# Performance work log

Hardware: AMD Instinct MI355X
Metric: run time of the kernel (lower is better)

The kernel has to match this reference:

```python
import jax, jax.numpy as jnp
import numpy as np

U = 100000   # num_users
I = 50000    # num_items
N = U + I    # total nodes
D = 64       # embed_size
L = 3        # n_layers
E = 2000000  # num edges
EPS = 1e-12  # F.normalize default eps


def setup_inputs() -> dict:
    key = jax.random.key(0)
    k1, k2, k3, k4 = jax.random.split(key, 4)
    user_emb = jax.random.normal(k1, (U, D), dtype=jnp.float32) * 0.1
    item_emb = jax.random.normal(k2, (I, D), dtype=jnp.float32) * 0.1
    rows = jax.random.randint(k3, (E,), 0, N, dtype=jnp.int32)
    cols = jax.random.randint(k4, (E,), 0, N, dtype=jnp.int32)
    return {"user_emb": user_emb, "item_emb": item_emb, "rows": rows, "cols": cols}


def _spmm(vals, rows, cols, x):
    # sparse [N,N] @ dense [N,D] via gather + segment reduce
    return jax.ops.segment_sum(vals[:, None] * x[cols], rows, num_segments=N)


def _l2norm(x):
    return x / jnp.maximum(jnp.linalg.norm(x, axis=1, keepdims=True), EPS)


def reference(user_emb, item_emb, rows, cols):
    emb0 = jnp.concatenate([user_emb, item_emb], axis=0)  # [N, D]

    # laplacian_adj: G = D^-1/2 A D^-1/2 on the same edge set
    deg = jax.ops.segment_sum(jnp.ones((E,), emb0.dtype), rows, num_segments=N)
    d_is = jnp.where(deg > 0, deg ** -0.5, 0.0)
    g_vals = d_is[rows] * d_is[cols]  # [E]

    cur = emb0
    acc = emb0
    user_fine, item_fine = [], []
    for _ in range(L):
        gnn = _spmm(g_vals, rows, cols, cur)  # [N, D]
        # fine_laplacian_adj: cosine-sim edge scores, row-normalized
        gr = _l2norm(gnn[rows])
        gc = _l2norm(gnn[cols])
        scores = (jnp.sum(gr * gc, axis=1) + 1.0) * 0.5  # [E] in [0,1]
        rowsum = jax.ops.segment_sum(scores, rows, num_segments=N)
        d_inv = jnp.where(rowsum > 0, 1.0 / rowsum, 0.0)
        fine = _spmm(d_inv[rows] * scores, rows, cols, cur)  # [N, D]
        cur = gnn + fine
        acc = acc + cur
        user_fine.append(fine[:U])
        item_fine.append(fine[U:])

    u_embs = acc[:U]
    i_embs = acc[U:]
    return (u_embs, i_embs, jnp.stack(user_fine, 0), jnp.stack(item_fine, 0))
```

## Files before the change

### kernel.cpp

```cpp
#include <hip/hip_runtime.h>

namespace {

typedef unsigned short u16;
typedef __attribute__((__ext_vector_type__(2))) float f32x2;
typedef __attribute__((__ext_vector_type__(4))) float f32x4;

constexpr int Un = 100000;
constexpr int In = 50000;
constexpr int Nn = 150000;
constexpr int D  = 64;
constexpr int Ln = 3;
constexpr int En = 2000000;
constexpr int CHUNK = 1024;
constexpr int NB = (Nn + CHUNK - 1) / CHUNK;
constexpr int DCAP = 128;
constexpr int NW = Nn / 8;

__device__ __forceinline__ u16 f2bf(float f) {
    unsigned u = __float_as_uint(f);
    unsigned r = (u + 0x7FFFu + ((u >> 16) & 1u)) >> 16;
    return (u16)r;
}
__device__ __forceinline__ float bflo(unsigned u) {
    return __uint_as_float(u << 16);
}
__device__ __forceinline__ float bfhi(unsigned u) {
    return __uint_as_float(u & 0xFFFF0000u);
}
__device__ __forceinline__ unsigned pack2(float lo, float hi) {
    return (unsigned)f2bf(lo) | ((unsigned)f2bf(hi) << 16);
}

__device__ __forceinline__ f32x2 pkfma(f32x2 a, f32x2 b, f32x2 c) {
    f32x2 d;
    asm("v_pk_fma_f32 %0, %1, %2, %3" : "=v"(d) : "v"(a), "v"(b), "v"(c));
    return d;
}
__device__ __forceinline__ f32x2 pkadd(f32x2 a, f32x2 b) {
    f32x2 d;
    asm("v_pk_add_f32 %0, %1, %2" : "=v"(d) : "v"(a), "v"(b));
    return d;
}

__device__ __forceinline__ float dpp_add8(float x) {
    x += __uint_as_float((unsigned)__builtin_amdgcn_update_dpp(
        0, (int)__float_as_uint(x), 0xB1, 0xF, 0xF, true));
    x += __uint_as_float((unsigned)__builtin_amdgcn_update_dpp(
        0, (int)__float_as_uint(x), 0x4E, 0xF, 0xF, true));
    x += __uint_as_float((unsigned)__builtin_amdgcn_update_dpp(
        0, (int)__float_as_uint(x), 0x141, 0xF, 0xF, true));
    return x;
}

__device__ __forceinline__ void unp8(uint4 q, f32x2* o) {
    o[0].x = bflo(q.x); o[0].y = bfhi(q.x);
    o[1].x = bflo(q.y); o[1].y = bfhi(q.y);
    o[2].x = bflo(q.z); o[2].y = bfhi(q.z);
    o[3].x = bflo(q.w); o[3].y = bfhi(q.w);
}

__global__ void count_kernel(const int* __restrict__ rows, int* __restrict__ deg,
                             int* __restrict__ eoff) {
    int e = blockIdx.x * blockDim.x + threadIdx.x;
    if (e < En) eoff[e] = atomicAdd(&deg[rows[e]], 1);
}

__global__ void scan_partial(const int* __restrict__ deg, float* __restrict__ d_is,
                             int* __restrict__ bsum) {
    int tid = threadIdx.x;
    int base = blockIdx.x * CHUNK + tid * 4;
    int s = 0;
#pragma unroll
    for (int i = 0; i < 4; ++i) {
        int idx = base + i;
        if (idx < Nn) {
            int d = deg[idx];
            s += d;
            d_is[idx] = d > 0 ? rsqrtf((float)d) : 0.f;
        }
    }
    __shared__ int sh[256];
    sh[tid] = s;
    __syncthreads();
    for (int o = 128; o > 0; o >>= 1) {
        if (tid < o) sh[tid] += sh[tid + o];
        __syncthreads();
    }
    if (tid == 0) bsum[blockIdx.x] = sh[0];
}

__global__ void scan_top(int* __restrict__ bsum, int* __restrict__ row_ptr) {
    __shared__ int sh[256];
    int tid = threadIdx.x;
    int v = (tid < NB) ? bsum[tid] : 0;
    sh[tid] = v;
    __syncthreads();
    for (int o = 1; o < 256; o <<= 1) {
        int t = (tid >= o) ? sh[tid - o] : 0;
        __syncthreads();
        sh[tid] += t;
        __syncthreads();
    }
    if (tid < NB) bsum[tid] = sh[tid] - v;
    if (tid == 255) row_ptr[Nn] = sh[255];
}

__global__ void scan_final(const int* __restrict__ deg, const int* __restrict__ bsum,
                           int* __restrict__ row_ptr) {
    int tid = threadIdx.x;
    int base = blockIdx.x * CHUNK + tid * 4;
    int v[4];
    int ts = 0;
#pragma unroll
    for (int i = 0; i < 4; ++i) {
        int idx = base + i;
        v[i] = (idx < Nn) ? deg[idx] : 0;
        ts += v[i];
    }
    __shared__ int sh[256];
    sh[tid] = ts;
    __syncthreads();
    for (int o = 1; o < 256; o <<= 1) {
        int t = (tid >= o) ? sh[tid - o] : 0;
        __syncthreads();
        sh[tid] += t;
        __syncthreads();
    }
    int excl = bsum[blockIdx.x] + sh[tid] - ts;
#pragma unroll
    for (int i = 0; i < 4; ++i) {
        int idx = base + i;
        if (idx < Nn) row_ptr[idx] = excl;
        excl += v[i];
    }
}

__global__ void fill_kernel(const int* __restrict__ rows, const int* __restrict__ cols,
                            const int* __restrict__ row_ptr, const int* __restrict__ eoff,
                            int* __restrict__ col_off) {
    int e = blockIdx.x * blockDim.x + threadIdx.x;
    if (e >= En) return;
    col_off[row_ptr[rows[e]] + eoff[e]] = cols[e] << 7;
}

__global__ void hist_part(const int* __restrict__ deg, int* __restrict__ hp) {
    __shared__ int lh[DCAP];
    int tid = threadIdx.x;
    if (tid < DCAP) lh[tid] = 0;
    __syncthreads();
    int base = blockIdx.x * CHUNK + tid * 4;
#pragma unroll
    for (int i = 0; i < 4; ++i) {
        int idx = base + i;
        if (idx < Nn) atomicAdd(&lh[min(deg[idx], DCAP - 1)], 1);
    }
    __syncthreads();
    if (tid < DCAP) hp[tid * NB + blockIdx.x] = lh[tid];
}

__global__ void hp_scan(int* __restrict__ hp) {
    constexpr int TOT = DCAP * NB;
    constexpr int PER = (TOT + 1023) / 1024;
    __shared__ int sh[1024];
    int tid = threadIdx.x;
    int base = tid * PER;
    int s = 0;
    for (int i = 0; i < PER; ++i) {
        int idx = base + i;
        if (idx < TOT) s += hp[idx];
    }
    sh[tid] = s;
    __syncthreads();
    for (int o = 1; o < 1024; o <<= 1) {
        int t = (tid >= o) ? sh[tid - o] : 0;
        __syncthreads();
        sh[tid] += t;
        __syncthreads();
    }
    int excl = sh[tid] - s;
    for (int i = 0; i < PER; ++i) {
        int idx = base + i;
        if (idx < TOT) {
            int v = hp[idx];
            hp[idx] = excl;
            excl += v;
        }
    }
}

__global__ void perm_scatter(const int* __restrict__ deg, const int* __restrict__ row_ptr,
                             const float* __restrict__ d_is, const int* __restrict__ hp,
                             int4* __restrict__ srt) {
    __shared__ int lh[DCAP];
    __shared__ int lbase[DCAP];
    int tid = threadIdx.x;
    if (tid < DCAP) lh[tid] = 0;
    __syncthreads();
    int base = blockIdx.x * CHUNK + tid * 4;
    int bin[4], rank[4];
#pragma unroll
    for (int i = 0; i < 4; ++i) {
        int idx = base + i;
        if (idx < Nn) {
            bin[i] = min(deg[idx], DCAP - 1);
            rank[i] = atomicAdd(&lh[bin[i]], 1);
        }
    }
    __syncthreads();
    if (tid < DCAP) lbase[tid] = hp[tid * NB + blockIdx.x];
    __syncthreads();
#pragma unroll
    for (int i = 0; i < 4; ++i) {
        int idx = base + i;
        if (idx < Nn) {
            int p = lbase[bin[i]] + rank[i];
            int4 v;
            v.x = row_ptr[idx];
            v.y = row_ptr[idx + 1];
            v.z = __float_as_int(d_is[idx]);
            v.w = idx;
            srt[p] = v;
        }
    }
}

__global__ void init_kernel(const float* __restrict__ ue, const float* __restrict__ ie,
                            const float* __restrict__ d_is,
                            float* __restrict__ out, u16* __restrict__ cur,
                            u16* __restrict__ S) {
    int i = (blockIdx.x * 256 + threadIdx.x) * 4;
    if (i >= Nn * D) return;
    const float* src = (i < Un * D) ? (ue + i) : (ie + (i - Un * D));
    float4 v = *(const float4*)src;
    *(float4*)(out + i) = v;
    ushort4 q;
    q.x = f2bf(v.x); q.y = f2bf(v.y); q.z = f2bf(v.z); q.w = f2bf(v.w);
    *(ushort4*)(cur + i) = q;
    float ds = d_is[i >> 6];
    ushort4 qs;
    qs.x = f2bf(v.x * ds); qs.y = f2bf(v.y * ds);
    qs.z = f2bf(v.z * ds); qs.w = f2bf(v.w * ds);
    *(ushort4*)(S + i) = qs;
}

__global__ __launch_bounds__(256) void spmm_gnn(const u16* __restrict__ S_,
                                                u16* __restrict__ Qn_,
                                                const int4* __restrict__ srt,
                                                const int* __restrict__ col_off,
                                                float* __restrict__ normv_s) {
    int w = (blockIdx.x * 256 + threadIdx.x) >> 6;
    if (w >= NW) return;
    int lane = threadIdx.x & 63;
    int g = lane >> 3, l = lane & 7;
    unsigned l16 = (unsigned)l * 16u;
    int wb = w * 8 + g;
    int4 q4 = srt[wb];
    int s = q4.x, t = q4.y;
    float dr = __int_as_float(q4.z);
    int r = q4.w;
    const char* pS = (const char*)S_;
    f32x2 z; z.x = 0.f; z.y = 0.f;
    f32x2 a2[4] = {z, z, z, z};
#pragma unroll 4
    for (int j = s; j < t; ++j) {
        unsigned off = (unsigned)col_off[j];
        uint4 q = *(const uint4*)(pS + (off + l16));
        f32x2 x2[4];
        unp8(q, x2);
#pragma unroll
        for (int p = 0; p < 4; ++p) a2[p] = pkadd(a2[p], x2[p]);
    }
    float sq = 0.f;
#pragma unroll
    for (int p = 0; p < 4; ++p) {
        sq = fmaf(a2[p].x, a2[p].x, sq);
        sq = fmaf(a2[p].y, a2[p].y, sq);
    }
    sq = dpp_add8(sq);
    float gn = dr * sqrtf(sq);
    float nrm = fmaxf(gn, 1e-12f);
    float scale = dr / nrm;
    if (l == 0) normv_s[wb] = nrm;
    unsigned ro = ((unsigned)r << 7) + l16;
    uint4 on;
    on.x = pack2(a2[0].x * scale, a2[0].y * scale);
    on.y = pack2(a2[1].x * scale, a2[1].y * scale);
    on.z = pack2(a2[2].x * scale, a2[2].y * scale);
    on.w = pack2(a2[3].x * scale, a2[3].y * scale);
    *(uint4*)((char*)Qn_ + ro) = on;
}

__global__ __launch_bounds__(256) void score_fine_kernel(const u16* __restrict__ A_,
                                                         const u16* __restrict__ Qn_,
                                                         u16* __restrict__ C_,
                                                         u16* __restrict__ S_,
                                                         const float* __restrict__ normv_s,
                                                         const int4* __restrict__ srt,
                                                         const int* __restrict__ col_off,
                                                         float* __restrict__ out, int layer) {
    int w = (blockIdx.x * 256 + threadIdx.x) >> 6;
    if (w >= NW) return;
    int lane = threadIdx.x & 63;
    int g = lane >> 3, l = lane & 7;
    unsigned l16 = (unsigned)l * 16u;
    int wb = w * 8 + g;
    int4 q4 = srt[wb];
    int s = q4.x, t = q4.y;
    float dsr = __int_as_float(q4.z);
    int r = q4.w;
    float nrm = normv_s[wb];
    const char* pQn = (const char*)Qn_;
    const char* pA  = (const char*)A_;
    unsigned ro = ((unsigned)r << 7) + l16;
    uint4 qbn = *(const uint4*)(pQn + ro);
    f32x2 b2[4];
    unp8(qbn, b2);
    f32x2 z; z.x = 0.f; z.y = 0.f;
    f32x2 facc[4] = {z, z, z, z};
    float rowsum = 0.f;
#pragma unroll 2
    for (int j = s; j < t; ++j) {
        unsigned off = (unsigned)col_off[j];
        unsigned vo = off + l16;
        uint4 qx = *(const uint4*)(pQn + vo);
        uint4 qy = *(const uint4*)(pA + vo);
        f32x2 x2[4];
        unp8(qx, x2);
        f32x2 d2 = pkfma(b2[0], x2[0], z);
        d2 = pkfma(b2[1], x2[1], d2);
        d2 = pkfma(b2[2], x2[2], d2);
        d2 = pkfma(b2[3], x2[3], d2);
        float d = dpp_add8(d2.x + d2.y);
        float sc = fmaf(d, 0.5f, 0.5f);
        rowsum += sc;
        f32x2 y2[4];
        unp8(qy, y2);
        f32x2 sc2; sc2.x = sc; sc2.y = sc;
#pragma unroll
        for (int p = 0; p < 4; ++p) facc[p] = pkfma(sc2, y2[p], facc[p]);
    }
    float di = rowsum > 0.f ? 1.f / rowsum : 0.f;
    float f[8] = {facc[0].x * di, facc[0].y * di, facc[1].x * di, facc[1].y * di,
                  facc[2].x * di, facc[2].y * di, facc[3].x * di, facc[3].y * di};
    float bb[8] = {b2[0].x, b2[0].y, b2[1].x, b2[1].y,
                   b2[2].x, b2[2].y, b2[3].x, b2[3].y};
    float cn[8];
#pragma unroll
    for (int k = 0; k < 8; ++k) cn[k] = fmaf(bb[k], nrm, f[k]);
    uint4 qn;
    qn.x = pack2(cn[0], cn[1]); qn.y = pack2(cn[2], cn[3]);
    qn.z = pack2(cn[4], cn[5]); qn.w = pack2(cn[6], cn[7]);
    *(uint4*)((char*)C_ + ro) = qn;
    if (layer != Ln - 1) {
        uint4 qs;
        qs.x = pack2(cn[0] * dsr, cn[1] * dsr);
        qs.y = pack2(cn[2] * dsr, cn[3] * dsr);
        qs.z = pack2(cn[4] * dsr, cn[5] * dsr);
        qs.w = pack2(cn[6] * dsr, cn[7] * dsr);
        *(uint4*)((char*)S_ + ro) = qs;
    }
    float* op = out + (size_t)r * D + l * 8;
    float4 a0 = ((float4*)op)[0], a1 = ((float4*)op)[1];
    a0.x += cn[0]; a0.y += cn[1]; a0.z += cn[2]; a0.w += cn[3];
    a1.x += cn[4]; a1.y += cn[5]; a1.z += cn[6]; a1.w += cn[7];
    ((float4*)op)[0] = a0;
    ((float4*)op)[1] = a1;
    size_t fo;
    if (r < Un)
        fo = (size_t)Nn * D + (size_t)layer * Un * D + (size_t)r * D + l * 8;
    else
        fo = (size_t)Nn * D + (size_t)Ln * Un * D + (size_t)layer * In * D
             + (size_t)(r - Un) * D + l * 8;
    f32x4 f0, f1;
    f0.x = f[0]; f0.y = f[1]; f0.z = f[2]; f0.w = f[3];
    f1.x = f[4]; f1.y = f[5]; f1.z = f[6]; f1.w = f[7];
    __builtin_nontemporal_store(f0, (f32x4*)(out + fo));
    __builtin_nontemporal_store(f1, (f32x4*)(out + fo) + 1);
}

}

extern "C" void kernel_launch(void* const* d_in, const int* in_sizes, int n_in,
                              void* d_out, int out_size, void* d_ws, size_t ws_size,
                              hipStream_t stream) {
    const float* user_emb = (const float*)d_in[0];
    const float* item_emb = (const float*)d_in[1];
    const int* rows = (const int*)d_in[2];
    const int* cols = (const int*)d_in[3];
    float* out = (float*)d_out;

    char* ws = (char*)d_ws;
    size_t off = 0;
    auto alloc = [&](size_t bytes) -> void* {
        void* p = ws + off;
        off += (bytes + 255) & ~size_t(255);
        return p;
    };
    u16*   buf0    = (u16*)  alloc((size_t)Nn * D * 2);
    u16*   buf1    = (u16*)  alloc((size_t)Nn * D * 2);
    u16*   buf2    = (u16*)  alloc((size_t)Nn * D * 2);
    u16*   buf3    = (u16*)  alloc((size_t)Nn * D * 2);
    int*   col_off = (int*)  alloc((size_t)(En + 8) * 4);
    int*   deg     = (int*)  alloc((size_t)Nn * 4);
    int*   row_ptr = (int*)  alloc((size_t)(Nn + 1) * 4);
    float* d_is    = (float*)alloc((size_t)Nn * 4);
    float* normv_s = (float*)alloc((size_t)Nn * 4);
    int4*  srt     = (int4*) alloc((size_t)Nn * 16);
    int*   hp      = (int*)  alloc((size_t)DCAP * NB * 4);
    int*   bsum    = (int*)  alloc(4096);
    int*   eoff    = (int*)buf2;
    (void)ws_size; (void)in_sizes; (void)n_in; (void)out_size;

    hipMemsetAsync(deg, 0, (size_t)Nn * 4, stream);

    const int EB = (En + 255) / 256;
    count_kernel<<<EB, 256, 0, stream>>>(rows, deg, eoff);
    scan_partial<<<NB, 256, 0, stream>>>(deg, d_is, bsum);
    scan_top<<<1, 256, 0, stream>>>(bsum, row_ptr);
    scan_final<<<NB, 256, 0, stream>>>(deg, bsum, row_ptr);
    hist_part<<<NB, 256, 0, stream>>>(deg, hp);
    hp_scan<<<1, 1024, 0, stream>>>(hp);
    fill_kernel<<<EB, 256, 0, stream>>>(rows, cols, row_ptr, eoff, col_off);
    perm_scatter<<<NB, 256, 0, stream>>>(deg, row_ptr, d_is, hp, srt);
    init_kernel<<<(Nn * D / 4 + 255) / 256, 256, 0, stream>>>(user_emb, item_emb, d_is,
                                                              out, buf0, buf3);

    const int WB = (NW * 64 + 255) / 256;
    u16* P = buf0;
    u16* R = buf1;
    u16* Qn = buf2;
    u16* S  = buf3;
    for (int l = 0; l < Ln; ++l) {
        spmm_gnn<<<WB, 256, 0, stream>>>(S, Qn, srt, col_off, normv_s);
        score_fine_kernel<<<WB, 256, 0, stream>>>(P, Qn, R, S, normv_s, srt,
                                                  col_off, out, l);
        u16* tmp = P; P = R; R = tmp;
    }
}
```

Measured before the change: 810.4 us.

## Interleave normalized-gnn and current embeddings per row and localize degree sort

Packs the normalized GNN output and the current embedding for each node into one 256-byte row, so the fine-aggregation loop reads both from adjacent cache lines at the same offset. The separate pre-scaled S buffer is dropped, and the spmm now scales each neighbor by d_is with an FMA instead of reading a prescaled copy. The global degree-histogram sort (hist_part and hp_scan) is replaced by a per-block sort inside perm_scatter, which removes two launches but only balances work within each 1024-node chunk. The cost is an extra scalar d_is gather per edge and a doubled per-row stride.

```diff
diff --git a/kernel.cpp b/kernel.cpp
--- a/kernel.cpp
+++ b/kernel.cpp
@@ -37,11 +37,6 @@
     asm("v_pk_fma_f32 %0, %1, %2, %3" : "=v"(d) : "v"(a), "v"(b), "v"(c));
     return d;
 }
-__device__ __forceinline__ f32x2 pkadd(f32x2 a, f32x2 b) {
-    f32x2 d;
-    asm("v_pk_add_f32 %0, %1, %2" : "=v"(d) : "v"(a), "v"(b));
-    return d;
-}
 
 __device__ __forceinline__ float dpp_add8(float x) {
     x += __uint_as_float((unsigned)__builtin_amdgcn_update_dpp(
@@ -141,59 +136,13 @@
                             int* __restrict__ col_off) {
     int e = blockIdx.x * blockDim.x + threadIdx.x;
     if (e >= En) return;
-    col_off[row_ptr[rows[e]] + eoff[e]] = cols[e] << 7;
-}
-
-__global__ void hist_part(const int* __restrict__ deg, int* __restrict__ hp) {
+    col_off[row_ptr[rows[e]] + eoff[e]] = cols[e] << 8;
+}
+
+__global__ void perm_scatter(const int* __restrict__ deg, const int* __restrict__ row_ptr,
+                             const float* __restrict__ d_is, int4* __restrict__ srt) {
     __shared__ int lh[DCAP];
-    int tid = threadIdx.x;
-    if (tid < DCAP) lh[tid] = 0;
-    __syncthreads();
-    int base = blockIdx.x * CHUNK + tid * 4;
-#pragma unroll
-    for (int i = 0; i < 4; ++i) {
-        int idx = base + i;
-        if (idx < Nn) atomicAdd(&lh[min(deg[idx], DCAP - 1)], 1);
-    }
-    __syncthreads();
-    if (tid < DCAP) hp[tid * NB + blockIdx.x] = lh[tid];
-}
-
-__global__ void hp_scan(int* __restrict__ hp) {
-    constexpr int TOT = DCAP * NB;
-    constexpr int PER = (TOT + 1023) / 1024;
-    __shared__ int sh[1024];
-    int tid = threadIdx.x;
-    int base = tid * PER;
-    int s = 0;
-    for (int i = 0; i < PER; ++i) {
-        int idx = base + i;
-        if (idx < TOT) s += hp[idx];
-    }
-    sh[tid] = s;
-    __syncthreads();
-    for (int o = 1; o < 1024; o <<= 1) {
-        int t = (tid >= o) ? sh[tid - o] : 0;
-        __syncthreads();
-        sh[tid] += t;
-        __syncthreads();
-    }
-    int excl = sh[tid] - s;
-    for (int i = 0; i < PER; ++i) {
-        int idx = base + i;
-        if (idx < TOT) {
-            int v = hp[idx];
-            hp[idx] = excl;
-            excl += v;
-        }
-    }
-}
-
-__global__ void perm_scatter(const int* __restrict__ deg, const int* __restrict__ row_ptr,
-                             const float* __restrict__ d_is, const int* __restrict__ hp,
-                             int4* __restrict__ srt) {
-    __shared__ int lh[DCAP];
-    __shared__ int lbase[DCAP];
+    __shared__ int sc[DCAP];
     int tid = threadIdx.x;
     if (tid < DCAP) lh[tid] = 0;
     __syncthreads();
@@ -208,13 +157,21 @@
         }
     }
     __syncthreads();
-    if (tid < DCAP) lbase[tid] = hp[tid * NB + blockIdx.x];
+    if (tid < DCAP) sc[tid] = lh[tid];
+    __syncthreads();
+    for (int o = 1; o < DCAP; o <<= 1) {
+        int t = (tid < DCAP && tid >= o) ? sc[tid - o] : 0;
+        __syncthreads();
+        if (tid < DCAP) sc[tid] += t;
+        __syncthreads();
+    }
+    if (tid < DCAP) sc[tid] -= lh[tid];
     __syncthreads();
 #pragma unroll
     for (int i = 0; i < 4; ++i) {
         int idx = base + i;
         if (idx < Nn) {
-            int p = lbase[bin[i]] + rank[i];
+            int p = blockIdx.x * CHUNK + sc[bin[i]] + rank[i];
             int4 v;
             v.x = row_ptr[idx];
             v.y = row_ptr[idx + 1];
@@ -226,28 +183,26 @@
 }
 
 __global__ void init_kernel(const float* __restrict__ ue, const float* __restrict__ ie,
-                            const float* __restrict__ d_is,
-                            float* __restrict__ out, u16* __restrict__ cur,
-                            u16* __restrict__ S) {
-    int i = (blockIdx.x * 256 + threadIdx.x) * 4;
-    if (i >= Nn * D) return;
-    const float* src = (i < Un * D) ? (ue + i) : (ie + (i - Un * D));
-    float4 v = *(const float4*)src;
-    *(float4*)(out + i) = v;
-    ushort4 q;
-    q.x = f2bf(v.x); q.y = f2bf(v.y); q.z = f2bf(v.z); q.w = f2bf(v.w);
-    *(ushort4*)(cur + i) = q;
-    float ds = d_is[i >> 6];
-    ushort4 qs;
-    qs.x = f2bf(v.x * ds); qs.y = f2bf(v.y * ds);
-    qs.z = f2bf(v.z * ds); qs.w = f2bf(v.w * ds);
-    *(ushort4*)(S + i) = qs;
-}
-
-__global__ __launch_bounds__(256) void spmm_gnn(const u16* __restrict__ S_,
-                                                u16* __restrict__ Qn_,
+                            float* __restrict__ out, u16* __restrict__ QA0) {
+    int i8 = (blockIdx.x * 256 + threadIdx.x) * 8;
+    if (i8 >= Nn * D) return;
+    const float* src = (i8 < Un * D) ? (ue + i8) : (ie + (i8 - Un * D));
+    float4 v0 = ((const float4*)src)[0];
+    float4 v1 = ((const float4*)src)[1];
+    ((float4*)(out + i8))[0] = v0;
+    ((float4*)(out + i8))[1] = v1;
+    unsigned r = (unsigned)(i8 >> 6);
+    unsigned dpos = (unsigned)(i8 & 63);
+    uint4 qa;
+    qa.x = pack2(v0.x, v0.y); qa.y = pack2(v0.z, v0.w);
+    qa.z = pack2(v1.x, v1.y); qa.w = pack2(v1.z, v1.w);
+    *(uint4*)((char*)QA0 + (r << 8) + 128u + dpos * 2u) = qa;
+}
+
+__global__ __launch_bounds__(256) void spmm_gnn(u16* __restrict__ QA,
                                                 const int4* __restrict__ srt,
                                                 const int* __restrict__ col_off,
+                                                const float* __restrict__ d_is,
                                                 float* __restrict__ normv_s) {
     int w = (blockIdx.x * 256 + threadIdx.x) >> 6;
     if (w >= NW) return;
@@ -259,17 +214,20 @@
     int s = q4.x, t = q4.y;
     float dr = __int_as_float(q4.z);
     int r = q4.w;
-    const char* pS = (const char*)S_;
+    const char* pQA = (const char*)QA;
+    const char* pd = (const char*)d_is;
     f32x2 z; z.x = 0.f; z.y = 0.f;
     f32x2 a2[4] = {z, z, z, z};
 #pragma unroll 4
     for (int j = s; j < t; ++j) {
         unsigned off = (unsigned)col_off[j];
-        uint4 q = *(const uint4*)(pS + (off + l16));
+        float dv = *(const float*)(pd + (off >> 6));
+        uint4 q = *(const uint4*)(pQA + (off + 128u + l16));
         f32x2 x2[4];
         unp8(q, x2);
-#pragma unroll
-        for (int p = 0; p < 4; ++p) a2[p] = pkadd(a2[p], x2[p]);
+        f32x2 v2; v2.x = dv; v2.y = dv;
+#pragma unroll
+        for (int p = 0; p < 4; ++p) a2[p] = pkfma(v2, x2[p], a2[p]);
     }
     float sq = 0.f;
 #pragma unroll
@@ -282,19 +240,17 @@
     float nrm = fmaxf(gn, 1e-12f);
     float scale = dr / nrm;
     if (l == 0) normv_s[wb] = nrm;
-    unsigned ro = ((unsigned)r << 7) + l16;
+    unsigned ro = ((unsigned)r << 8) + l16;
     uint4 on;
     on.x = pack2(a2[0].x * scale, a2[0].y * scale);
     on.y = pack2(a2[1].x * scale, a2[1].y * scale);
     on.z = pack2(a2[2].x * scale, a2[2].y * scale);
     on.w = pack2(a2[3].x * scale, a2[3].y * scale);
-    *(uint4*)((char*)Qn_ + ro) = on;
-}
-
-__global__ __launch_bounds__(256) void score_fine_kernel(const u16* __restrict__ A_,
-                                                         const u16* __restrict__ Qn_,
-                                                         u16* __restrict__ C_,
-                                                         u16* __restrict__ S_,
+    *(uint4*)((char*)QA + ro) = on;
+}
+
+__global__ __launch_bounds__(256) void score_fine_kernel(const u16* __restrict__ QAc,
+                                                         u16* __restrict__ QAn,
                                                          const float* __restrict__ normv_s,
                                                          const int4* __restrict__ srt,
                                                          const int* __restrict__ col_off,
@@ -307,24 +263,22 @@
     int wb = w * 8 + g;
     int4 q4 = srt[wb];
     int s = q4.x, t = q4.y;
-    float dsr = __int_as_float(q4.z);
     int r = q4.w;
     float nrm = normv_s[wb];
-    const char* pQn = (const char*)Qn_;
-    const char* pA  = (const char*)A_;
-    unsigned ro = ((unsigned)r << 7) + l16;
-    uint4 qbn = *(const uint4*)(pQn + ro);
+    const char* pQA = (const char*)QAc;
+    unsigned ro = ((unsigned)r << 8) + l16;
+    uint4 qbn = *(const uint4*)(pQA + ro);
     f32x2 b2[4];
     unp8(qbn, b2);
     f32x2 z; z.x = 0.f; z.y = 0.f;
     f32x2 facc[4] = {z, z, z, z};
     float rowsum = 0.f;
-#pragma unroll 2
+#pragma unroll 4
     for (int j = s; j < t; ++j) {
         unsigned off = (unsigned)col_off[j];
         unsigned vo = off + l16;
-        uint4 qx = *(const uint4*)(pQn + vo);
-        uint4 qy = *(const uint4*)(pA + vo);
+        uint4 qx = *(const uint4*)(pQA + vo);
+        uint4 qy = *(const uint4*)(pQA + vo + 128u);
         f32x2 x2[4];
         unp8(qx, x2);
         f32x2 d2 = pkfma(b2[0], x2[0], z);
@@ -351,15 +305,7 @@
     uint4 qn;
     qn.x = pack2(cn[0], cn[1]); qn.y = pack2(cn[2], cn[3]);
     qn.z = pack2(cn[4], cn[5]); qn.w = pack2(cn[6], cn[7]);
-    *(uint4*)((char*)C_ + ro) = qn;
-    if (layer != Ln - 1) {
-        uint4 qs;
-        qs.x = pack2(cn[0] * dsr, cn[1] * dsr);
-        qs.y = pack2(cn[2] * dsr, cn[3] * dsr);
-        qs.z = pack2(cn[4] * dsr, cn[5] * dsr);
-        qs.w = pack2(cn[6] * dsr, cn[7] * dsr);
-        *(uint4*)((char*)S_ + ro) = qs;
-    }
+    *(uint4*)((char*)QAn + ro + 128u) = qn;
     float* op = out + (size_t)r * D + l * 8;
     float4 a0 = ((float4*)op)[0], a1 = ((float4*)op)[1];
     a0.x += cn[0]; a0.y += cn[1]; a0.z += cn[2]; a0.w += cn[3];
@@ -397,19 +343,16 @@
         off += (bytes + 255) & ~size_t(255);
         return p;
     };
-    u16*   buf0    = (u16*)  alloc((size_t)Nn * D * 2);
-    u16*   buf1    = (u16*)  alloc((size_t)Nn * D * 2);
-    u16*   buf2    = (u16*)  alloc((size_t)Nn * D * 2);
-    u16*   buf3    = (u16*)  alloc((size_t)Nn * D * 2);
+    u16*   QA0     = (u16*)  alloc((size_t)Nn * 256);
+    u16*   QA1     = (u16*)  alloc((size_t)Nn * 256);
     int*   col_off = (int*)  alloc((size_t)(En + 8) * 4);
     int*   deg     = (int*)  alloc((size_t)Nn * 4);
     int*   row_ptr = (int*)  alloc((size_t)(Nn + 1) * 4);
     float* d_is    = (float*)alloc((size_t)Nn * 4);
     float* normv_s = (float*)alloc((size_t)Nn * 4);
     int4*  srt     = (int4*) alloc((size_t)Nn * 16);
-    int*   hp      = (int*)  alloc((size_t)DCAP * NB * 4);
     int*   bsum    = (int*)  alloc(4096);
-    int*   eoff    = (int*)buf2;
+    int*   eoff    = (int*)QA1;
     (void)ws_size; (void)in_sizes; (void)n_in; (void)out_size;
 
     hipMemsetAsync(deg, 0, (size_t)Nn * 4, stream);
@@ -419,22 +362,18 @@
     scan_partial<<<NB, 256, 0, stream>>>(deg, d_is, bsum);
     scan_top<<<1, 256, 0, stream>>>(bsum, row_ptr);
     scan_final<<<NB, 256, 0, stream>>>(deg, bsum, row_ptr);
-    hist_part<<<NB, 256, 0, stream>>>(deg, hp);
-    hp_scan<<<1, 1024, 0, stream>>>(hp);
     fill_kernel<<<EB, 256, 0, stream>>>(rows, cols, row_ptr, eoff, col_off);
-    perm_scatter<<<NB, 256, 0, stream>>>(deg, row_ptr, d_is, hp, srt);
-    init_kernel<<<(Nn * D / 4 + 255) / 256, 256, 0, stream>>>(user_emb, item_emb, d_is,
-                                                              out, buf0, buf3);
+    perm_scatter<<<NB, 256, 0, stream>>>(deg, row_ptr, d_is, srt);
+    init_kernel<<<(Nn * D / 8 + 255) / 256, 256, 0, stream>>>(user_emb, item_emb,
+                                                              out, QA0);
 
     const int WB = (NW * 64 + 255) / 256;
-    u16* P = buf0;
-    u16* R = buf1;
-    u16* Qn = buf2;
-    u16* S  = buf3;
+    u16* Pq = QA0;
+    u16* Nq = QA1;
     for (int l = 0; l < Ln; ++l) {
-        spmm_gnn<<<WB, 256, 0, stream>>>(S, Qn, srt, col_off, normv_s);
-        score_fine_kernel<<<WB, 256, 0, stream>>>(P, Qn, R, S, normv_s, srt,
+        spmm_gnn<<<WB, 256, 0, stream>>>(Pq, srt, col_off, d_is, normv_s);
+        score_fine_kernel<<<WB, 256, 0, stream>>>(Pq, Nq, normv_s, srt,
                                                   col_off, out, l);
-        u16* tmp = P; P = R; R = tmp;
-    }
-}
+        u16* tmp = Pq; Pq = Nq; Nq = tmp;
+    }
+}
```

After: 840.5 us. 3.7% more time.
